# Kernel optimization log

Hardware: AMD Instinct MI355X
Metric: run time of the kernel (lower is better)

The kernel has to match this reference:

```python
import jax, jax.numpy as jnp
import numpy as np

B, D, E, H, C, TOPK = 4096, 768, 16, 768, 1000, 4

def setup_inputs() -> dict:
    key = jax.random.key(0)
    ks = jax.random.split(key, 4)
    s_in = 1.0 / np.sqrt(D)
    return {
        'features': jax.random.normal(ks[0], (B, D), dtype=jnp.float32),
        'router_w': jax.random.normal(ks[1], (D, E), dtype=jnp.float32) * s_in,
        'router_b': jnp.zeros((E,), jnp.float32),
        'ln_g': jnp.ones((E, D), jnp.float32),
        'ln_b': jnp.zeros((E, D), jnp.float32),
        'w1': jax.random.normal(ks[2], (E, D, H), dtype=jnp.float32) * s_in,
        'b1': jnp.zeros((E, H), jnp.float32),
        'w2': jax.random.normal(ks[3], (E, H, C), dtype=jnp.float32) * (1.0 / np.sqrt(H)),
        'b2': jnp.zeros((E, C), jnp.float32),
    }

def reference(features, router_w, router_b, ln_g, ln_b, w1, b1, w2, b2):
    # router
    gate_logits = features @ router_w + router_b          # [B,E]
    gate_probs = jax.nn.softmax(gate_logits, axis=-1)
    topk_vals, topk_idx = jax.lax.top_k(gate_probs, TOPK)  # [B,K]
    topk_vals = topk_vals / jnp.sum(topk_vals, axis=-1, keepdims=True)

    # all experts computed densely: LayerNorm (per-expert affine) -> Linear -> GELU -> Linear
    mu = jnp.mean(features, axis=-1, keepdims=True)
    var = jnp.mean((features - mu) ** 2, axis=-1, keepdims=True)
    xn = (features - mu) / jnp.sqrt(var + 1e-5)            # [B,D]
    y = xn[:, None, :] * ln_g[None, :, :] + ln_b[None, :, :]  # [B,E,D]
    h = jax.nn.gelu(jnp.einsum('bed,edh->beh', y, w1) + b1[None], approximate=False)  # [B,E,H]
    all_logits = jnp.einsum('beh,ehc->bec', h, w2) + b2[None]  # [B,E,C]

    # top-k gather + weighted softmax mixture
    selected = jnp.take_along_axis(all_logits, topk_idx[:, :, None], axis=1)  # [B,K,C]
    market_probs = jnp.sum(topk_vals[:, :, None] * jax.nn.softmax(selected, axis=-1), axis=1)  # [B,C]
    all_probs = jax.nn.softmax(jnp.transpose(all_logits, (1, 0, 2)), axis=-1)  # [E,B,C]
    return market_probs, all_probs, gate_probs
```

## Files before the change

### kernel.cpp

```cpp
#include <hip/hip_runtime.h>
#include <hip/hip_bf16.h>
#include <cmath>

#define B_ 4096
#define D_ 768
#define E_ 16
#define H_ 768
#define C_ 1000
#define CP_ 1024
#define K_ 768

typedef __bf16 bf16_t;
typedef __bf16 bf16x8 __attribute__((ext_vector_type(8)));
typedef float f32x4 __attribute__((ext_vector_type(4)));

__device__ __forceinline__ void async_lds16(const void* g, void* l) {
  __builtin_amdgcn_global_load_lds(
      (const __attribute__((address_space(1))) void*)g,
      (__attribute__((address_space(3))) void*)l, 16, 0, 0);
}

__global__ __launch_bounds__(256) void k_router(
    const float* __restrict__ feat, const float* __restrict__ rw,
    const float* __restrict__ rb, float* __restrict__ gate_out,
    int* __restrict__ tk_idx, float* __restrict__ tk_val) {
  int w = threadIdx.x >> 6, lane = threadIdx.x & 63;
  int b = blockIdx.x * 4 + w;
  float acc[E_];
#pragma unroll
  for (int e = 0; e < E_; ++e) acc[e] = 0.f;
  const float* frow = feat + (size_t)b * D_;
#pragma unroll
  for (int it = 0; it < D_ / 64; ++it) {
    int d = it * 64 + lane;
    float f = frow[d];
    const float4* r4 = reinterpret_cast<const float4*>(rw + (size_t)d * E_);
    float4 q0 = r4[0], q1 = r4[1], q2 = r4[2], q3 = r4[3];
    acc[0]  += f * q0.x; acc[1]  += f * q0.y; acc[2]  += f * q0.z; acc[3]  += f * q0.w;
    acc[4]  += f * q1.x; acc[5]  += f * q1.y; acc[6]  += f * q1.z; acc[7]  += f * q1.w;
    acc[8]  += f * q2.x; acc[9]  += f * q2.y; acc[10] += f * q2.z; acc[11] += f * q2.w;
    acc[12] += f * q3.x; acc[13] += f * q3.y; acc[14] += f * q3.z; acc[15] += f * q3.w;
  }
#pragma unroll
  for (int e = 0; e < E_; ++e) {
#pragma unroll
    for (int off = 32; off; off >>= 1) acc[e] += __shfl_xor(acc[e], off);
    acc[e] += rb[e];
  }
  if (lane == 0) {
    float mx = acc[0];
#pragma unroll
    for (int e = 1; e < E_; ++e) mx = fmaxf(mx, acc[e]);
    float p[E_];
    float s = 0.f;
#pragma unroll
    for (int e = 0; e < E_; ++e) { p[e] = expf(acc[e] - mx); s += p[e]; }
    float inv = 1.f / s;
    float* go = gate_out + (size_t)b * E_;
#pragma unroll
    for (int e = 0; e < E_; ++e) { p[e] *= inv; go[e] = p[e]; }
    float lg[E_];
#pragma unroll
    for (int e = 0; e < E_; ++e) lg[e] = acc[e];
    int idx4[4]; float v4[4]; float vs = 0.f;
#pragma unroll
    for (int k = 0; k < 4; ++k) {
      int bi = 0; float bv = -1e30f;
#pragma unroll
      for (int e = 0; e < E_; ++e) { if (lg[e] > bv) { bv = lg[e]; bi = e; } }
      idx4[k] = bi; v4[k] = p[bi]; vs += p[bi]; lg[bi] = -1e30f;
    }
    float nv = 1.f / vs;
#pragma unroll
    for (int k = 0; k < 4; ++k) { tk_idx[b * 4 + k] = idx4[k]; tk_val[b * 4 + k] = v4[k] * nv; }
  }
}

__global__ __launch_bounds__(256) void k_ln(const float* __restrict__ feat,
                                            bf16_t* __restrict__ xn) {
  int w = threadIdx.x >> 6, lane = threadIdx.x & 63;
  int b = blockIdx.x * 4 + w;
  const float* x = feat + (size_t)b * D_;
  float v[D_ / 64];
  float s = 0.f, sq = 0.f;
#pragma unroll
  for (int i = 0; i < D_ / 64; ++i) {
    v[i] = x[i * 64 + lane];
    s += v[i]; sq += v[i] * v[i];
  }
#pragma unroll
  for (int off = 32; off; off >>= 1) { s += __shfl_xor(s, off); sq += __shfl_xor(sq, off); }
  float mu = s * (1.f / D_);
  float var = sq * (1.f / D_) - mu * mu;
  float rs = rsqrtf(var + 1e-5f);
  bf16_t* o = xn + (size_t)b * D_;
#pragma unroll
  for (int i = 0; i < D_ / 64; ++i)
    o[i * 64 + lane] = (bf16_t)((v[i] - mu) * rs);
}

__global__ void k_tw1(const float* __restrict__ w1, const float* __restrict__ lng,
                      bf16_t* __restrict__ w1T) {
  __shared__ float t[32][33];
  int e = blockIdx.z, dT = blockIdx.y * 32, hT = blockIdx.x * 32;
  int tx = threadIdx.x, ty = threadIdx.y;
  const float* w1e = w1 + (size_t)e * D_ * H_;
  const float* ge = lng + (size_t)e * D_;
#pragma unroll
  for (int r = 0; r < 4; ++r) {
    int d = dT + ty + r * 8;
    t[ty + r * 8][tx] = w1e[(size_t)d * H_ + hT + tx] * ge[d];
  }
  __syncthreads();
  bf16_t* o = w1T + (size_t)e * H_ * D_;
#pragma unroll
  for (int r = 0; r < 4; ++r) {
    int h = hT + ty + r * 8;
    o[(size_t)h * D_ + dT + tx] = (bf16_t)t[tx][ty + r * 8];
  }
}

__global__ void k_tw2(const float* __restrict__ w2, bf16_t* __restrict__ w2T) {
  __shared__ float t[32][33];
  int e = blockIdx.z, hT = blockIdx.y * 32, cT = blockIdx.x * 32;
  int tx = threadIdx.x, ty = threadIdx.y;
  const float* w2e = w2 + (size_t)e * H_ * C_;
#pragma unroll
  for (int r = 0; r < 4; ++r) {
    int h = hT + ty + r * 8, c = cT + tx;
    t[ty + r * 8][tx] = (c < C_) ? w2e[(size_t)h * C_ + c] : 0.f;
  }
  __syncthreads();
  bf16_t* o = w2T + (size_t)e * CP_ * H_;
#pragma unroll
  for (int r = 0; r < 4; ++r) {
    int c = cT + ty + r * 8;
    o[(size_t)c * H_ + hT + tx] = (bf16_t)t[tx][ty + r * 8];
  }
}

__global__ __launch_bounds__(256) void k_bias_part(const float* __restrict__ w1,
                                                   const float* __restrict__ lnb,
                                                   float* __restrict__ pb) {
  int e = blockIdx.z, z = blockIdx.y;
  int h = blockIdx.x * 256 + threadIdx.x;
  const float* w1e = w1 + (size_t)e * D_ * H_;
  const float* lb = lnb + (size_t)e * D_;
  float acc = 0.f;
  int d0 = z * (D_ / 8);
#pragma unroll 8
  for (int d = d0; d < d0 + D_ / 8; ++d) acc += lb[d] * w1e[(size_t)d * H_ + h];
  pb[((size_t)e * 8 + z) * H_ + h] = acc;
}

__global__ __launch_bounds__(256) void k_bias_comb(const float* __restrict__ b1,
                                                   const float* __restrict__ pb,
                                                   float* __restrict__ bias1) {
  int e = blockIdx.y;
  int h = blockIdx.x * 256 + threadIdx.x;
  float a = b1[(size_t)e * H_ + h];
#pragma unroll
  for (int z = 0; z < 8; ++z) a += pb[((size_t)e * 8 + z) * H_ + h];
  bias1[(size_t)e * H_ + h] = a;
}

template <int MODE>
__global__ __launch_bounds__(256) void k_gemm(
    const bf16_t* __restrict__ Abase, size_t aStride,
    const bf16_t* __restrict__ Bt, int Np,
    const float* __restrict__ bias,
    bf16_t* __restrict__ outb, float* __restrict__ outf) {
  __shared__ __attribute__((aligned(16))) bf16_t As[128 * 32];
  __shared__ __attribute__((aligned(16))) bf16_t Bs[128 * 32];
  int e = blockIdx.z;
  int m0 = blockIdx.y * 128, n0 = blockIdx.x * 128;
  const bf16_t* A = Abase + (size_t)e * aStride;
  const bf16_t* Be = Bt + ((size_t)e * Np + n0) * K_;
  int tid = threadIdx.x;
  int lane = tid & 63, w = tid >> 6;
  int wm = (w & 1) * 64, wn = (w >> 1) * 64;
  int fr = lane & 15, fk = (lane >> 4) * 8;

  f32x4 acc[4][4];
#pragma unroll
  for (int i = 0; i < 4; ++i)
#pragma unroll
    for (int j = 0; j < 4; ++j) acc[i][j] = f32x4{0.f, 0.f, 0.f, 0.f};

  int r0 = tid >> 2;
  int c0 = (tid & 3) * 8;
  const bf16_t* a_src0 = A + (size_t)(m0 + r0) * K_ + c0;
  const bf16_t* a_src1 = A + (size_t)(m0 + r0 + 64) * K_ + c0;
  const bf16_t* b_src0 = Be + (size_t)r0 * K_ + c0;
  const bf16_t* b_src1 = Be + (size_t)(r0 + 64) * K_ + c0;
  bf16_t* a_dst0 = As + tid * 8;
  bf16_t* a_dst1 = As + 2048 + tid * 8;
  bf16_t* b_dst0 = Bs + tid * 8;
  bf16_t* b_dst1 = Bs + 2048 + tid * 8;

  for (int kk = 0; kk < K_; kk += 32) {
    async_lds16(a_src0 + kk, a_dst0);
    async_lds16(a_src1 + kk, a_dst1);
    async_lds16(b_src0 + kk, b_dst0);
    async_lds16(b_src1 + kk, b_dst1);
    __syncthreads();
    bf16x8 afr[4], bfr[4];
#pragma unroll
    for (int i = 0; i < 4; ++i)
      afr[i] = *(const bf16x8*)&As[(wm + i * 16 + fr) * 32 + fk];
#pragma unroll
    for (int i = 0; i < 4; ++i)
      bfr[i] = *(const bf16x8*)&Bs[(wn + i * 16 + fr) * 32 + fk];
#pragma unroll
    for (int i = 0; i < 4; ++i)
#pragma unroll
      for (int j = 0; j < 4; ++j)
        acc[i][j] = __builtin_amdgcn_mfma_f32_16x16x32_bf16(afr[i], bfr[j], acc[i][j], 0, 0, 0);
    __syncthreads();
  }

  int rbse = (lane >> 4) * 4;
  int cl = lane & 15;
#pragma unroll
  for (int i = 0; i < 4; ++i) {
#pragma unroll
    for (int j = 0; j < 4; ++j) {
      int n = n0 + wn + j * 16 + cl;
      if (MODE == 0) {
        float bs = bias[(size_t)e * H_ + n];
#pragma unroll
        for (int r = 0; r < 4; ++r) {
          int m = m0 + wm + i * 16 + rbse + r;
          float v = acc[i][j][r] + bs;
          v = 0.5f * v * (1.f + erff(v * 0.70710678118654752f));
          outb[((size_t)e * B_ + m) * H_ + n] = (bf16_t)v;
        }
      } else {
        if (n < C_) {
          float bs = bias[(size_t)e * C_ + n];
#pragma unroll
          for (int r = 0; r < 4; ++r) {
            int m = m0 + wm + i * 16 + rbse + r;
            outf[((size_t)e * B_ + m) * C_ + n] = acc[i][j][r] + bs;
          }
        }
      }
    }
  }
}

__global__ __launch_bounds__(256) void k_softmax(float* __restrict__ p) {
  int w = threadIdx.x >> 6, lane = threadIdx.x & 63;
  size_t r = (size_t)blockIdx.x * 4 + w;
  float* row = p + r * C_;
  float4* row4 = reinterpret_cast<float4*>(row);
  const int n4 = C_ / 4;
  float4 v[4];
  float mx = -1e30f;
#pragma unroll
  for (int i = 0; i < 4; ++i) {
    int idx = i * 64 + lane;
    if (idx < n4) {
      v[i] = row4[idx];
      mx = fmaxf(mx, fmaxf(fmaxf(v[i].x, v[i].y), fmaxf(v[i].z, v[i].w)));
    }
  }
#pragma unroll
  for (int off = 32; off; off >>= 1) mx = fmaxf(mx, __shfl_xor(mx, off));
  float s = 0.f;
#pragma unroll
  for (int i = 0; i < 4; ++i) {
    int idx = i * 64 + lane;
    if (idx < n4) {
      v[i].x = __expf(v[i].x - mx); v[i].y = __expf(v[i].y - mx);
      v[i].z = __expf(v[i].z - mx); v[i].w = __expf(v[i].w - mx);
      s += v[i].x + v[i].y + v[i].z + v[i].w;
    }
  }
#pragma unroll
  for (int off = 32; off; off >>= 1) s += __shfl_xor(s, off);
  float inv = 1.f / s;
#pragma unroll
  for (int i = 0; i < 4; ++i) {
    int idx = i * 64 + lane;
    if (idx < n4) {
      v[i].x *= inv; v[i].y *= inv; v[i].z *= inv; v[i].w *= inv;
      row4[idx] = v[i];
    }
  }
}

__global__ __launch_bounds__(256) void k_market(const float* __restrict__ allp,
                                                const int* __restrict__ tki,
                                                const float* __restrict__ tkv,
                                                float* __restrict__ out0) {
  int b = blockIdx.y;
  int c = blockIdx.x * 256 + threadIdx.x;
  if (c >= C_) return;
  const int* ix = tki + (size_t)b * 4;
  const float* vv = tkv + (size_t)b * 4;
  float s = 0.f;
#pragma unroll
  for (int k = 0; k < 4; ++k)
    s += vv[k] * allp[((size_t)ix[k] * B_ + b) * C_ + c];
  out0[(size_t)b * C_ + c] = s;
}

extern "C" void kernel_launch(void* const* d_in, const int* in_sizes, int n_in,
                              void* d_out, int out_size, void* d_ws, size_t ws_size,
                              hipStream_t stream) {
  const float* feat = (const float*)d_in[0];
  const float* rw   = (const float*)d_in[1];
  const float* rb   = (const float*)d_in[2];
  const float* lng  = (const float*)d_in[3];
  const float* lnb  = (const float*)d_in[4];
  const float* w1   = (const float*)d_in[5];
  const float* b1   = (const float*)d_in[6];
  const float* w2   = (const float*)d_in[7];
  const float* b2   = (const float*)d_in[8];

  float* out0 = (float*)d_out;
  float* out1 = out0 + (size_t)B_ * C_;
  float* out2 = out1 + (size_t)E_ * B_ * C_;

  char* ws = (char*)d_ws;
  size_t off = 0;
  auto take = [&](size_t bytes) -> void* {
    void* p = ws + off;
    off += (bytes + 255) & ~(size_t)255;
    return p;
  };
  bf16_t* xn   = (bf16_t*)take((size_t)B_ * D_ * 2);
  bf16_t* w1T  = (bf16_t*)take((size_t)E_ * H_ * D_ * 2);
  bf16_t* w2T  = (bf16_t*)take((size_t)E_ * CP_ * H_ * 2);
  float* bias1 = (float*)take((size_t)E_ * H_ * 4);
  float* pb    = (float*)take((size_t)E_ * 8 * H_ * 4);
  int* tki     = (int*)take((size_t)B_ * 4 * 4);
  float* tkv   = (float*)take((size_t)B_ * 4 * 4);
  bf16_t* Hact = (bf16_t*)take((size_t)E_ * B_ * H_ * 2);

  k_router<<<B_ / 4, 256, 0, stream>>>(feat, rw, rb, out2, tki, tkv);
  k_ln<<<B_ / 4, 256, 0, stream>>>(feat, xn);
  k_tw1<<<dim3(24, 24, E_), dim3(32, 8), 0, stream>>>(w1, lng, w1T);
  k_tw2<<<dim3(32, 24, E_), dim3(32, 8), 0, stream>>>(w2, w2T);
  k_bias_part<<<dim3(3, 8, E_), 256, 0, stream>>>(w1, lnb, pb);
  k_bias_comb<<<dim3(3, E_), 256, 0, stream>>>(b1, pb, bias1);
  k_gemm<0><<<dim3(6, 32, E_), 256, 0, stream>>>(xn, 0, w1T, H_, bias1, Hact, nullptr);
  k_gemm<1><<<dim3(8, 32, E_), 256, 0, stream>>>(Hact, (size_t)B_ * H_, w2T, CP_, b2, nullptr, out1);
  k_softmax<<<(E_ * B_) / 4, 256, 0, stream>>>(out1);
  k_market<<<dim3(4, B_), 256, 0, stream>>>(out1, tki, tkv, out0);
}
```

Before: 821.9 us.

## Fuse router+LN, fold bias into transpose, remap GEMM grid per XCD, bf16 logits

Merges the router and LayerNorm kernels so features are read once. The LN-bias contribution is folded into the w1 transpose kernel through atomics, which removes two bias kernels. GEMM blocks are remapped from a flat 1-D grid so each XCD handles whole experts, aiming for better L2 reuse of weights. When workspace allows, the second GEMM writes bf16 logits to a scratch buffer and a new softmax reads them, cutting fp32 round-trip traffic on the large logits tensor. The cost is lower precision of the logits before softmax, and atomic float adds make the bias order nondeterministic.

```diff
diff --git a/kernel.cpp b/kernel.cpp
--- a/kernel.cpp
+++ b/kernel.cpp
@@ -20,20 +20,24 @@
       (__attribute__((address_space(3))) void*)l, 16, 0, 0);
 }
 
-__global__ __launch_bounds__(256) void k_router(
+__global__ __launch_bounds__(256) void k_router_ln(
     const float* __restrict__ feat, const float* __restrict__ rw,
     const float* __restrict__ rb, float* __restrict__ gate_out,
-    int* __restrict__ tk_idx, float* __restrict__ tk_val) {
+    int* __restrict__ tk_idx, float* __restrict__ tk_val,
+    bf16_t* __restrict__ xn) {
   int w = threadIdx.x >> 6, lane = threadIdx.x & 63;
   int b = blockIdx.x * 4 + w;
   float acc[E_];
 #pragma unroll
   for (int e = 0; e < E_; ++e) acc[e] = 0.f;
   const float* frow = feat + (size_t)b * D_;
+  float v[D_ / 64];
+  float s = 0.f, sq = 0.f;
 #pragma unroll
   for (int it = 0; it < D_ / 64; ++it) {
     int d = it * 64 + lane;
     float f = frow[d];
+    v[it] = f; s += f; sq += f * f;
     const float4* r4 = reinterpret_cast<const float4*>(rw + (size_t)d * E_);
     float4 q0 = r4[0], q1 = r4[1], q2 = r4[2], q3 = r4[3];
     acc[0]  += f * q0.x; acc[1]  += f * q0.y; acc[2]  += f * q0.z; acc[3]  += f * q0.w;
@@ -42,81 +46,85 @@
     acc[12] += f * q3.x; acc[13] += f * q3.y; acc[14] += f * q3.z; acc[15] += f * q3.w;
   }
 #pragma unroll
-  for (int e = 0; e < E_; ++e) {
-#pragma unroll
-    for (int off = 32; off; off >>= 1) acc[e] += __shfl_xor(acc[e], off);
-    acc[e] += rb[e];
-  }
-  if (lane == 0) {
-    float mx = acc[0];
-#pragma unroll
-    for (int e = 1; e < E_; ++e) mx = fmaxf(mx, acc[e]);
-    float p[E_];
-    float s = 0.f;
-#pragma unroll
-    for (int e = 0; e < E_; ++e) { p[e] = expf(acc[e] - mx); s += p[e]; }
-    float inv = 1.f / s;
-    float* go = gate_out + (size_t)b * E_;
-#pragma unroll
-    for (int e = 0; e < E_; ++e) { p[e] *= inv; go[e] = p[e]; }
-    float lg[E_];
-#pragma unroll
-    for (int e = 0; e < E_; ++e) lg[e] = acc[e];
-    int idx4[4]; float v4[4]; float vs = 0.f;
-#pragma unroll
-    for (int k = 0; k < 4; ++k) {
-      int bi = 0; float bv = -1e30f;
-#pragma unroll
-      for (int e = 0; e < E_; ++e) { if (lg[e] > bv) { bv = lg[e]; bi = e; } }
-      idx4[k] = bi; v4[k] = p[bi]; vs += p[bi]; lg[bi] = -1e30f;
-    }
-    float nv = 1.f / vs;
-#pragma unroll
-    for (int k = 0; k < 4; ++k) { tk_idx[b * 4 + k] = idx4[k]; tk_val[b * 4 + k] = v4[k] * nv; }
-  }
-}
-
-__global__ __launch_bounds__(256) void k_ln(const float* __restrict__ feat,
-                                            bf16_t* __restrict__ xn) {
-  int w = threadIdx.x >> 6, lane = threadIdx.x & 63;
-  int b = blockIdx.x * 4 + w;
-  const float* x = feat + (size_t)b * D_;
-  float v[D_ / 64];
-  float s = 0.f, sq = 0.f;
-#pragma unroll
-  for (int i = 0; i < D_ / 64; ++i) {
-    v[i] = x[i * 64 + lane];
-    s += v[i]; sq += v[i] * v[i];
-  }
-#pragma unroll
   for (int off = 32; off; off >>= 1) { s += __shfl_xor(s, off); sq += __shfl_xor(sq, off); }
   float mu = s * (1.f / D_);
   float var = sq * (1.f / D_) - mu * mu;
   float rs = rsqrtf(var + 1e-5f);
   bf16_t* o = xn + (size_t)b * D_;
 #pragma unroll
-  for (int i = 0; i < D_ / 64; ++i)
-    o[i * 64 + lane] = (bf16_t)((v[i] - mu) * rs);
+  for (int it = 0; it < D_ / 64; ++it)
+    o[it * 64 + lane] = (bf16_t)((v[it] - mu) * rs);
+#pragma unroll
+  for (int e = 0; e < E_; ++e) {
+#pragma unroll
+    for (int off = 32; off; off >>= 1) acc[e] += __shfl_xor(acc[e], off);
+    acc[e] += rb[e];
+  }
+  if (lane == 0) {
+    float mx = acc[0];
+#pragma unroll
+    for (int e = 1; e < E_; ++e) mx = fmaxf(mx, acc[e]);
+    float p[E_]; float ps = 0.f;
+#pragma unroll
+    for (int e = 0; e < E_; ++e) { p[e] = expf(acc[e] - mx); ps += p[e]; }
+    float inv = 1.f / ps;
+    float* go = gate_out + (size_t)b * E_;
+#pragma unroll
+    for (int e = 0; e < E_; ++e) { p[e] *= inv; go[e] = p[e]; }
+    float lg[E_];
+#pragma unroll
+    for (int e = 0; e < E_; ++e) lg[e] = acc[e];
+    int idx4[4]; float v4[4]; float vs = 0.f;
+#pragma unroll
+    for (int k = 0; k < 4; ++k) {
+      int bi = 0; float bv = -1e30f;
+#pragma unroll
+      for (int e = 0; e < E_; ++e) { if (lg[e] > bv) { bv = lg[e]; bi = e; } }
+      idx4[k] = bi; v4[k] = p[bi]; vs += p[bi]; lg[bi] = -1e30f;
+    }
+    float nv = 1.f / vs;
+#pragma unroll
+    for (int k = 0; k < 4; ++k) { tk_idx[b * 4 + k] = idx4[k]; tk_val[b * 4 + k] = v4[k] * nv; }
+  }
+}
+
+__global__ __launch_bounds__(256) void k_bias_init(const float* __restrict__ b1,
+                                                   float* __restrict__ bias1) {
+  int i = blockIdx.x * 256 + threadIdx.x;
+  bias1[i] = b1[i];
 }
 
 __global__ void k_tw1(const float* __restrict__ w1, const float* __restrict__ lng,
-                      bf16_t* __restrict__ w1T) {
+                      const float* __restrict__ lnb, bf16_t* __restrict__ w1T,
+                      float* __restrict__ bias1) {
   __shared__ float t[32][33];
+  __shared__ float br[8][33];
   int e = blockIdx.z, dT = blockIdx.y * 32, hT = blockIdx.x * 32;
   int tx = threadIdx.x, ty = threadIdx.y;
   const float* w1e = w1 + (size_t)e * D_ * H_;
   const float* ge = lng + (size_t)e * D_;
+  const float* lb = lnb + (size_t)e * D_;
+  float bsum = 0.f;
 #pragma unroll
   for (int r = 0; r < 4; ++r) {
     int d = dT + ty + r * 8;
-    t[ty + r * 8][tx] = w1e[(size_t)d * H_ + hT + tx] * ge[d];
-  }
+    float val = w1e[(size_t)d * H_ + hT + tx];
+    t[ty + r * 8][tx] = val * ge[d];
+    bsum += lb[d] * val;
+  }
+  br[ty][tx] = bsum;
   __syncthreads();
   bf16_t* o = w1T + (size_t)e * H_ * D_;
 #pragma unroll
   for (int r = 0; r < 4; ++r) {
     int h = hT + ty + r * 8;
     o[(size_t)h * D_ + dT + tx] = (bf16_t)t[tx][ty + r * 8];
+  }
+  if (ty == 0) {
+    float a = 0.f;
+#pragma unroll
+    for (int z = 0; z < 8; ++z) a += br[z][tx];
+    atomicAdd(&bias1[(size_t)e * H_ + hT + tx], a);
   }
 }
 
@@ -139,32 +147,7 @@
   }
 }
 
-__global__ __launch_bounds__(256) void k_bias_part(const float* __restrict__ w1,
-                                                   const float* __restrict__ lnb,
-                                                   float* __restrict__ pb) {
-  int e = blockIdx.z, z = blockIdx.y;
-  int h = blockIdx.x * 256 + threadIdx.x;
-  const float* w1e = w1 + (size_t)e * D_ * H_;
-  const float* lb = lnb + (size_t)e * D_;
-  float acc = 0.f;
-  int d0 = z * (D_ / 8);
-#pragma unroll 8
-  for (int d = d0; d < d0 + D_ / 8; ++d) acc += lb[d] * w1e[(size_t)d * H_ + h];
-  pb[((size_t)e * 8 + z) * H_ + h] = acc;
-}
-
-__global__ __launch_bounds__(256) void k_bias_comb(const float* __restrict__ b1,
-                                                   const float* __restrict__ pb,
-                                                   float* __restrict__ bias1) {
-  int e = blockIdx.y;
-  int h = blockIdx.x * 256 + threadIdx.x;
-  float a = b1[(size_t)e * H_ + h];
-#pragma unroll
-  for (int z = 0; z < 8; ++z) a += pb[((size_t)e * 8 + z) * H_ + h];
-  bias1[(size_t)e * H_ + h] = a;
-}
-
-template <int MODE>
+template <int MODE, int NT>
 __global__ __launch_bounds__(256) void k_gemm(
     const bf16_t* __restrict__ Abase, size_t aStride,
     const bf16_t* __restrict__ Bt, int Np,
@@ -172,8 +155,13 @@
     bf16_t* __restrict__ outb, float* __restrict__ outf) {
   __shared__ __attribute__((aligned(16))) bf16_t As[128 * 32];
   __shared__ __attribute__((aligned(16))) bf16_t Bs[128 * 32];
-  int e = blockIdx.z;
-  int m0 = blockIdx.y * 128, n0 = blockIdx.x * 128;
+  int id = blockIdx.x;
+  int xcd = id & 7, seq = id >> 3;
+  const int PER_E = 32 * NT;
+  int e = xcd * (E_ / 8) + seq / PER_E;
+  int rem = seq % PER_E;
+  int m0 = (rem / NT) * 128, n0 = (rem % NT) * 128;
+
   const bf16_t* A = Abase + (size_t)e * aStride;
   const bf16_t* Be = Bt + ((size_t)e * Np + n0) * K_;
   int tid = threadIdx.x;
@@ -231,9 +219,16 @@
 #pragma unroll
         for (int r = 0; r < 4; ++r) {
           int m = m0 + wm + i * 16 + rbse + r;
-          float v = acc[i][j][r] + bs;
-          v = 0.5f * v * (1.f + erff(v * 0.70710678118654752f));
-          outb[((size_t)e * B_ + m) * H_ + n] = (bf16_t)v;
+          float vv = acc[i][j][r] + bs;
+          vv = 0.5f * vv * (1.f + erff(vv * 0.70710678118654752f));
+          outb[((size_t)e * B_ + m) * H_ + n] = (bf16_t)vv;
+        }
+      } else if (MODE == 1) {
+        float bs = (n < C_) ? bias[(size_t)e * C_ + n] : 0.f;
+#pragma unroll
+        for (int r = 0; r < 4; ++r) {
+          int m = m0 + wm + i * 16 + rbse + r;
+          outb[((size_t)e * B_ + m) * CP_ + n] = (bf16_t)(acc[i][j][r] + bs);
         }
       } else {
         if (n < C_) {
@@ -245,6 +240,49 @@
           }
         }
       }
+    }
+  }
+}
+
+__global__ __launch_bounds__(256) void k_softmax_b(const bf16_t* __restrict__ lg,
+                                                   float* __restrict__ out1) {
+  int w = threadIdx.x >> 6, lane = threadIdx.x & 63;
+  size_t r = (size_t)blockIdx.x * 4 + w;
+  const bf16_t* row = lg + r * CP_;
+  float f[2][8];
+  float mx = -1e30f;
+#pragma unroll
+  for (int it = 0; it < 2; ++it) {
+    int ch = it * 64 + lane;
+    bf16x8 x = *(const bf16x8*)(row + ch * 8);
+    if (ch < 125) {
+#pragma unroll
+      for (int q = 0; q < 8; ++q) { f[it][q] = (float)x[q]; mx = fmaxf(mx, f[it][q]); }
+    }
+  }
+#pragma unroll
+  for (int off = 32; off; off >>= 1) mx = fmaxf(mx, __shfl_xor(mx, off));
+  float s = 0.f;
+#pragma unroll
+  for (int it = 0; it < 2; ++it) {
+    int ch = it * 64 + lane;
+    if (ch < 125) {
+#pragma unroll
+      for (int q = 0; q < 8; ++q) { f[it][q] = __expf(f[it][q] - mx); s += f[it][q]; }
+    }
+  }
+#pragma unroll
+  for (int off = 32; off; off >>= 1) s += __shfl_xor(s, off);
+  float inv = 1.f / s;
+  float* orow = out1 + r * C_;
+#pragma unroll
+  for (int it = 0; it < 2; ++it) {
+    int ch = it * 64 + lane;
+    if (ch < 125) {
+      float4 a = make_float4(f[it][0] * inv, f[it][1] * inv, f[it][2] * inv, f[it][3] * inv);
+      float4 b = make_float4(f[it][4] * inv, f[it][5] * inv, f[it][6] * inv, f[it][7] * inv);
+      *(float4*)(orow + ch * 8) = a;
+      *(float4*)(orow + ch * 8 + 4) = b;
     }
   }
 }
@@ -334,19 +372,24 @@
   bf16_t* w1T  = (bf16_t*)take((size_t)E_ * H_ * D_ * 2);
   bf16_t* w2T  = (bf16_t*)take((size_t)E_ * CP_ * H_ * 2);
   float* bias1 = (float*)take((size_t)E_ * H_ * 4);
-  float* pb    = (float*)take((size_t)E_ * 8 * H_ * 4);
   int* tki     = (int*)take((size_t)B_ * 4 * 4);
   float* tkv   = (float*)take((size_t)B_ * 4 * 4);
   bf16_t* Hact = (bf16_t*)take((size_t)E_ * B_ * H_ * 2);
-
-  k_router<<<B_ / 4, 256, 0, stream>>>(feat, rw, rb, out2, tki, tkv);
-  k_ln<<<B_ / 4, 256, 0, stream>>>(feat, xn);
-  k_tw1<<<dim3(24, 24, E_), dim3(32, 8), 0, stream>>>(w1, lng, w1T);
+  size_t logit_bytes = (size_t)E_ * B_ * CP_ * 2;
+  bool use_b16_logits = (off + logit_bytes) <= ws_size;
+  bf16_t* logitsB = use_b16_logits ? (bf16_t*)take(logit_bytes) : nullptr;
+
+  k_router_ln<<<B_ / 4, 256, 0, stream>>>(feat, rw, rb, out2, tki, tkv, xn);
+  k_bias_init<<<E_ * H_ / 256, 256, 0, stream>>>(b1, bias1);
+  k_tw1<<<dim3(24, 24, E_), dim3(32, 8), 0, stream>>>(w1, lng, lnb, w1T, bias1);
   k_tw2<<<dim3(32, 24, E_), dim3(32, 8), 0, stream>>>(w2, w2T);
-  k_bias_part<<<dim3(3, 8, E_), 256, 0, stream>>>(w1, lnb, pb);
-  k_bias_comb<<<dim3(3, E_), 256, 0, stream>>>(b1, pb, bias1);
-  k_gemm<0><<<dim3(6, 32, E_), 256, 0, stream>>>(xn, 0, w1T, H_, bias1, Hact, nullptr);
-  k_gemm<1><<<dim3(8, 32, E_), 256, 0, stream>>>(Hact, (size_t)B_ * H_, w2T, CP_, b2, nullptr, out1);
-  k_softmax<<<(E_ * B_) / 4, 256, 0, stream>>>(out1);
+  k_gemm<0, 6><<<E_ * 32 * 6, 256, 0, stream>>>(xn, 0, w1T, H_, bias1, Hact, nullptr);
+  if (use_b16_logits) {
+    k_gemm<1, 8><<<E_ * 32 * 8, 256, 0, stream>>>(Hact, (size_t)B_ * H_, w2T, CP_, b2, logitsB, nullptr);
+    k_softmax_b<<<(E_ * B_) / 4, 256, 0, stream>>>(logitsB, out1);
+  } else {
+    k_gemm<2, 8><<<E_ * 32 * 8, 256, 0, stream>>>(Hact, (size_t)B_ * H_, w2T, CP_, b2, nullptr, out1);
+    k_softmax<<<(E_ * B_) / 4, 256, 0, stream>>>(out1);
+  }
   k_market<<<dim3(4, B_), 256, 0, stream>>>(out1, tki, tkv, out0);
 }
```

New measurement: 705.7 us. -14.1%, faster.
